# Performance work log

Measured on AMD Instinct MI355X. Metric: run time of the kernel, lower is better.

Reference implementation:

```python
import jax, jax.numpy as jnp
import numpy as np

# dims: batch, seq_len, d_model, heads, head_dim, n_buckets
B, L, DM, H, DH, K = 4, 4096, 1024, 16, 64, 8
C = L // K            # chunk length after bucket sort (512); extra_len==0 for these dims
CS = 0.1              # cluster_score mixing weight


def setup_inputs() -> dict:
    key = jax.random.key(0)
    ks = jax.random.split(key, 12)
    s = 0.02
    def p(k, shape):
        return jax.random.normal(k, shape, jnp.float32) * s
    return {
        "inputs_q": jax.random.normal(ks[0], (B, L, DM), jnp.float32),
        "wq": p(ks[1], (DM, H, DH)), "bq": jnp.zeros((H, DH), jnp.float32),
        "wk": p(ks[2], (DM, H, DH)), "bk": jnp.zeros((H, DH), jnp.float32),
        "wv": p(ks[3], (DM, H, DH)), "bv": jnp.zeros((H, DH), jnp.float32),
        "w_shared": p(ks[4], (H, DH, K)),
        "w_qscore": p(ks[5], (H, DH, K)),
        "w_kscore": p(ks[6], (H, DH, K)),
        "wo": p(ks[7], (H, DH, DM)), "bo": jnp.zeros((DM,), jnp.float32),
    }


def reference(inputs_q, wq, bq, wk, bk, wv, bv, w_shared, w_qscore, w_kscore, wo, bo):
    scale = 1.0 / np.sqrt(DH)
    # QKV projections (DenseGeneral to (H, DH))
    q = jnp.einsum('bld,dhk->blhk', inputs_q, wq) + bq  # [B,L,H,DH]
    k = jnp.einsum('bld,dhk->blhk', inputs_q, wk) + bk
    v = jnp.einsum('bld,dhk->blhk', inputs_q, wv) + bv

    # learned linear cluster scores on stop-gradient q/k
    mix_q = (1.0 - CS) * w_shared + CS * w_qscore  # [H,DH,K]
    mix_k = (1.0 - CS) * w_shared + CS * w_kscore
    qs = jnp.einsum('blhd,hdk->blhk', jax.lax.stop_gradient(q), mix_q)  # [B,L,H,K]
    ksc = jnp.einsum('blhd,hdk->blhk', jax.lax.stop_gradient(k), mix_k)

    # bucket assignment = argmax learned score; per-(batch,head) stable sort by bucket id
    bq_id = jnp.argmax(qs, -1).transpose(0, 2, 1)   # [B,H,L]
    bk_id = jnp.argmax(ksc, -1).transpose(0, 2, 1)
    sort_q = jnp.argsort(bq_id, axis=-1)            # stable in jax
    sort_k = jnp.argsort(bk_id, axis=-1)

    qh = q.transpose(0, 2, 1, 3)  # [B,H,L,DH]
    kh = k.transpose(0, 2, 1, 3)
    vh = v.transpose(0, 2, 1, 3)
    sq = jnp.take_along_axis(qh, sort_q[..., None], axis=2).reshape(B, H, K, C, DH)
    sk = jnp.take_along_axis(kh, sort_k[..., None], axis=2).reshape(B, H, K, C, DH)
    sv = jnp.take_along_axis(vh, sort_k[..., None], axis=2).reshape(B, H, K, C, DH)

    # block attention within each bucket chunk
    logits = jnp.einsum('bhncd,bhned->bhnce', sq, sk) * scale  # [B,H,K,C,C]
    attn = jax.nn.softmax(logits, axis=-1)
    o = jnp.einsum('bhnce,bhned->bhncd', attn, sv).reshape(B, H, L, DH)

    # unsort back to original token order
    inv_q = jnp.argsort(sort_q, axis=-1)
    o = jnp.take_along_axis(o, inv_q[..., None], axis=2)  # [B,H,L,DH]
    o = o.transpose(0, 2, 1, 3)                            # [B,L,H,DH]

    out = jnp.einsum('blhd,hdo->blo', o, wo) + bo          # output projection

    # auxiliary load-balancing routing loss over buckets (extra_loss)
    p_q = jax.nn.softmax(qs, -1)
    p_k = jax.nn.softmax(ksc, -1)
    f_q = jax.nn.one_hot(jnp.argmax(qs, -1), K, dtype=qs.dtype)
    f_k = jax.nn.one_hot(jnp.argmax(ksc, -1), K, dtype=qs.dtype)
    lq = K * jnp.mean(jnp.sum(jnp.mean(f_q, 1) * jnp.mean(p_q, 1), -1))
    lk = K * jnp.mean(jnp.sum(jnp.mean(f_k, 1) * jnp.mean(p_k, 1), -1))
    extra_loss = 0.5 * (lq + lk)
    return out, extra_loss
```

## Files before the change

kernel.cpp:

```cpp
#include <hip/hip_runtime.h>
#include <hip/hip_bf16.h>

#define BB 4
#define LL 4096
#define DM 1024
#define HH 16
#define DHD 64
#define KB 8
#define BL 16384
#define FLAGCAP 131072

typedef __attribute__((ext_vector_type(8))) short short8;
typedef __attribute__((ext_vector_type(4))) short short4v;
typedef __attribute__((ext_vector_type(4))) float float4v;

#define MFMA16(A, Bx, C) __builtin_amdgcn_mfma_f32_16x16x32_bf16(A, Bx, C, 0, 0, 0)

static __device__ __forceinline__ short bf16s(float f) {
  __hip_bfloat16 h = __float2bfloat16(f);
  return *reinterpret_cast<short*>(&h);
}
static __device__ __forceinline__ float b2f(short s) {
  __hip_bfloat16 h = *reinterpret_cast<__hip_bfloat16*>(&s);
  return __bfloat162float(h);
}
static __device__ __forceinline__ void gl16(const void* g, void* l) {
  __builtin_amdgcn_global_load_lds(
      (const __attribute__((address_space(1))) void*)g,
      (__attribute__((address_space(3))) void*)l, 16, 0, 0);
}

__global__ __launch_bounds__(256) void prep_wt(const float* __restrict__ wq,
                                               const float* __restrict__ wk,
                                               const float* __restrict__ wv,
                                               const float* __restrict__ wo,
                                               __hip_bfloat16* __restrict__ wt_qkv,
                                               __hip_bfloat16* __restrict__ wt_o) {
  int blk = blockIdx.x;
  int s = blk >> 8;
  int rem = blk & 255;
  int k0 = (rem >> 4) * 64;
  int n0 = (rem & 15) * 64;
  const float* src = (s == 0) ? wq : (s == 1) ? wk : (s == 2) ? wv : wo;
  __hip_bfloat16* dst = (s < 3) ? (wt_qkv + (size_t)s * 1024 * 1024) : wt_o;
  __shared__ float ls[64][65];
  int t = threadIdx.x;
#pragma unroll
  for (int p = 0; p < 4; ++p) {
    int sid = p * 256 + t;
    int r = sid >> 4, c4 = sid & 15;
    float4 v = *reinterpret_cast<const float4*>(src + (size_t)(k0 + r) * 1024 + n0 + c4 * 4);
    ls[r][c4 * 4 + 0] = v.x; ls[r][c4 * 4 + 1] = v.y;
    ls[r][c4 * 4 + 2] = v.z; ls[r][c4 * 4 + 3] = v.w;
  }
  __syncthreads();
#pragma unroll
  for (int p = 0; p < 4; ++p) {
    int sid = p * 256 + t;
    int n = sid >> 4, kq = sid & 15;
    short4v pk;
#pragma unroll
    for (int j = 0; j < 4; ++j) pk[j] = bf16s(ls[kq * 4 + j][n]);
    *reinterpret_cast<short4v*>(dst + (size_t)(n0 + n) * 1024 + k0 + kq * 4) = pk;
  }
}

__global__ __launch_bounds__(256) void prep_wsc(const float* __restrict__ wq,
                                                const float* __restrict__ wk,
                                                const float* __restrict__ wsh,
                                                const float* __restrict__ wqs,
                                                const float* __restrict__ wks,
                                                const float* __restrict__ bq,
                                                const float* __restrict__ bk,
                                                double* __restrict__ wscg,
                                                double* __restrict__ bsc,
                                                __hip_bfloat16* __restrict__ whb,
                                                __hip_bfloat16* __restrict__ wmb) {
  int col = blockIdx.x;
  int side = col >> 7, h = (col >> 3) & 15, kk = col & 7;
  int g = side * 16 + h;
  const float* w = side ? wk : wq;
  const float* wscore = side ? wks : wqs;
  __shared__ double mix[64];
  int t = threadIdx.x;
  if (t < 64)
    mix[t] = 0.9 * (double)wsh[(h * 64 + t) * 8 + kk] +
             0.1 * (double)wscore[(h * 64 + t) * 8 + kk];
  __syncthreads();
#pragma unroll
  for (int p = 0; p < 4; ++p) {
    int d = p * 256 + t;
    double acc = 0.0;
    const float* wr = w + (size_t)d * 1024 + h * 64;
#pragma unroll
    for (int j = 0; j < 64; ++j) acc += (double)wr[j] * mix[j];
    wscg[((size_t)g * 1024 + d) * 8 + kk] = acc;
    short hi = bf16s((float)acc);
    short mid = bf16s((float)(acc - (double)b2f(hi)));
    *reinterpret_cast<short*>(whb + (size_t)col * 1024 + d) = hi;
    *reinterpret_cast<short*>(wmb + (size_t)col * 1024 + d) = mid;
  }
  if (t == 0) {
    const float* br = (side ? bk : bq) + h * 64;
    double acc = 0.0;
    for (int j = 0; j < 64; ++j) acc += (double)br[j] * mix[j];
    bsc[col] = acc;
  }
}

__global__ __launch_bounds__(512) void score_gemm(const float* __restrict__ x,
                                                  const __hip_bfloat16* __restrict__ whb,
                                                  const __hip_bfloat16* __restrict__ wmb,
                                                  const double* __restrict__ bsc,
                                                  __hip_bfloat16* __restrict__ xb,
                                                  int* __restrict__ bid,
                                                  float* __restrict__ psumg,
                                                  int* __restrict__ flagcnt,
                                                  int* __restrict__ list) {
  __shared__ char sm[147456];
  int t = threadIdx.x;
  int m0 = blockIdx.x * 64;
  int lane = t & 63;
  int wu = __builtin_amdgcn_readfirstlane(t >> 6);
  int lm = lane & 15, quad = lane >> 4;
  int wmr = (wu & 1) * 32, wn = (wu >> 1) * 64;
  int rb = wu * 32, rr = lane >> 3, phys = lane & 7;
  int am = t >> 3, akc = t & 7;

  auto STAGEB = [&](int bufsel, int k0) {
    char* base = sm + 16384 + bufsel * 65536;
#pragma unroll
    for (int p = 0; p < 4; ++p) {
      int row = rb + p * 8 + rr;
      int kc = (phys - row) & 7;
      gl16(whb + (size_t)row * 1024 + k0 + kc * 8, base + (rb + p * 8) * 128);
      gl16(wmb + (size_t)row * 1024 + k0 + kc * 8, base + 32768 + (rb + p * 8) * 128);
    }
  };

  float4 xf0, xf1;
  auto LOADX = [&](int k0) {
    const float* ap = x + (size_t)(m0 + am) * 1024 + k0 + akc * 8;
    xf0 = *reinterpret_cast<const float4*>(ap);
    xf1 = *reinterpret_cast<const float4*>(ap + 4);
  };

  STAGEB(0, 0);
  LOADX(0);

  float4v zero = {0.f, 0.f, 0.f, 0.f};
  float4v acc[2][4];
#pragma unroll
  for (int i = 0; i < 2; ++i)
#pragma unroll
    for (int j = 0; j < 4; ++j) acc[i][j] = zero;

#pragma unroll 1
  for (int kt = 0; kt < 16; ++kt) {
    int k0 = kt * 64;
    short8 hi, lo;
    {
      float vv[8] = {xf0.x, xf0.y, xf0.z, xf0.w, xf1.x, xf1.y, xf1.z, xf1.w};
#pragma unroll
      for (int e = 0; e < 8; ++e) {
        short h = bf16s(vv[e]);
        hi[e] = h;
        lo[e] = bf16s(vv[e] - b2f(h));
      }
    }
    asm volatile("" ::: "memory");
    __builtin_amdgcn_s_barrier();
    asm volatile("" ::: "memory");
    *reinterpret_cast<short8*>(sm + am * 128 + ((akc + am) & 7) * 16) = hi;
    *reinterpret_cast<short8*>(sm + 8192 + am * 128 + ((akc + am) & 7) * 16) = lo;
    *reinterpret_cast<short8*>(xb + (size_t)(m0 + am) * 1024 + k0 + akc * 8) = hi;
    if (kt < 15) {
      STAGEB((kt + 1) & 1, k0 + 64);
      LOADX(k0 + 64);
    }
    asm volatile("s_waitcnt lgkmcnt(0)" ::: "memory");
    __builtin_amdgcn_s_barrier();
    asm volatile("" ::: "memory");

    const char* bb = sm + 16384 + (kt & 1) * 65536;
#pragma unroll
    for (int kh = 0; kh < 2; ++kh) {
      short8 ah[2], al[2], bh[4], bm[4];
#pragma unroll
      for (int i = 0; i < 2; ++i) {
        int row = wmr + i * 16 + lm;
        int ph = ((kh * 4 + quad) + row) & 7;
        ah[i] = *reinterpret_cast<const short8*>(sm + row * 128 + ph * 16);
        al[i] = *reinterpret_cast<const short8*>(sm + 8192 + row * 128 + ph * 16);
      }
#pragma unroll
      for (int j = 0; j < 4; ++j) {
        int rn = wn + j * 16 + lm;
        int ph = ((kh * 4 + quad) + rn) & 7;
        bh[j] = *reinterpret_cast<const short8*>(bb + rn * 128 + ph * 16);
        bm[j] = *reinterpret_cast<const short8*>(bb + 32768 + rn * 128 + ph * 16);
      }
#pragma unroll
      for (int i = 0; i < 2; ++i)
#pragma unroll
        for (int j = 0; j < 4; ++j) {
          acc[i][j] = MFMA16(ah[i], bh[j], acc[i][j]);
          acc[i][j] = MFMA16(ah[i], bm[j], acc[i][j]);
          acc[i][j] = MFMA16(al[i], bh[j], acc[i][j]);
        }
    }
  }

  int b = m0 >> 12;
  int l0 = m0 & 4095;
  int kk = lm & 7;
#pragma unroll
  for (int j = 0; j < 4; ++j) {
    int n = wn + j * 16 + lm;
    int g = n >> 3;
    int side = g >> 4, h = g & 15;
    int slab = (side * 4 + b) * 16 + h;
    float bias = (float)bsc[n];
    float pp = 0.f;
#pragma unroll
    for (int i = 0; i < 2; ++i)
#pragma unroll
      for (int r = 0; r < 4; ++r) {
        float v = acc[i][j][r] + bias;
        float bmx = v; int bi = kk;
#pragma unroll
        for (int o = 1; o < 8; o <<= 1) {
          float vo = __shfl_xor(bmx, o);
          int io = __shfl_xor(bi, o);
          if (vo > bmx || (vo == bmx && io < bi)) { bmx = vo; bi = io; }
        }
        float vm = (kk == bi) ? -3.0e38f : v;
#pragma unroll
        for (int o = 1; o < 8; o <<= 1) vm = fmaxf(vm, __shfl_xor(vm, o));
        float e = __expf(v - bmx);
        float es = e;
#pragma unroll
        for (int o = 1; o < 8; o <<= 1) es += __shfl_xor(es, o);
        pp += e * (1.f / es);
        int l = l0 + wmr + i * 16 + quad * 4 + r;
        if (kk == 0) {
          bid[(slab << 12) | l] = bi;
          if (bmx - vm < 5e-4f) {
            int pos = atomicAdd(flagcnt, 1);
            if (pos < FLAGCAP) list[pos] = (slab << 12) | l;
          }
        }
      }
    pp += __shfl_xor(pp, 16);
    pp += __shfl_xor(pp, 32);
    if (quad == 0) atomicAdd(&psumg[slab * 8 + kk], pp);
  }
}

__global__ __launch_bounds__(256) void refine_kernel(const float* __restrict__ x,
                                                     const double* __restrict__ wscg,
                                                     const double* __restrict__ bsc,
                                                     const int* __restrict__ flagcnt,
                                                     const int* __restrict__ list,
                                                     int* __restrict__ bid) {
  int lane = threadIdx.x & 63;
  int w = threadIdx.x >> 6;
  int cnt = flagcnt[0];
  if (cnt > FLAGCAP) cnt = FLAGCAP;
  for (int i = blockIdx.x * 4 + w; i < cnt; i += 1024) {
    int e = list[i];
    int slab = e >> 12, l = e & 4095;
    int side = slab >> 6, b = (slab >> 4) & 3, h = slab & 15;
    int g = side * 16 + h;
    int row = b * 4096 + l;
    double acc[8] = {0, 0, 0, 0, 0, 0, 0, 0};
    const float* xr = x + (size_t)row * 1024 + lane * 16;
    const double* wr = wscg + ((size_t)g * 1024 + lane * 16) * 8;
#pragma unroll
    for (int dd = 0; dd < 16; ++dd) {
      double xv = (double)xr[dd];
#pragma unroll
      for (int j = 0; j < 8; ++j) acc[j] += xv * wr[dd * 8 + j];
    }
#pragma unroll
    for (int j = 0; j < 8; ++j) {
      double v = acc[j];
      v += __shfl_xor(v, 32); v += __shfl_xor(v, 16); v += __shfl_xor(v, 8);
      v += __shfl_xor(v, 4);  v += __shfl_xor(v, 2);  v += __shfl_xor(v, 1);
      acc[j] = v + bsc[g * 8 + j];
    }
    if (lane == 0) {
      double mx = acc[0]; int am = 0;
#pragma unroll
      for (int j = 1; j < 8; ++j) { if (acc[j] > mx) { mx = acc[j]; am = j; } }
      bid[(slab << 12) | l] = am;
    }
  }
}

__global__ __launch_bounds__(256) void sort_kernel(const int* __restrict__ bid,
                                                   int* __restrict__ sortq,
                                                   int* __restrict__ sortk,
                                                   int* __restrict__ cntg) {
  int blk = blockIdx.x;
  int side = blk >> 6, b = (blk >> 4) & 3, h = blk & 15;
  const int* ids = bid + (((side * 4 + b) * 16 + h) << 12);
  int* outp = (side ? sortk : sortq) + ((b * 16 + h) << 12);
  __shared__ int cnt[8][257];
  __shared__ int base[8];
  int t = threadIdx.x;
  int loc[16];
  int hist[8] = {0, 0, 0, 0, 0, 0, 0, 0};
#pragma unroll
  for (int j = 0; j < 16; ++j) { loc[j] = ids[t * 16 + j] & 7; hist[loc[j]]++; }
#pragma unroll
  for (int k = 0; k < 8; ++k) cnt[k][t + 1] = hist[k];
  if (t < 8) cnt[t][0] = 0;
  __syncthreads();
  if (t < 8) {
    for (int i = 1; i <= 256; ++i) cnt[t][i] += cnt[t][i - 1];
  }
  __syncthreads();
  if (t == 0) {
    int run = 0;
    for (int k = 0; k < 8; ++k) { base[k] = run; run += cnt[k][256]; }
  }
  if (t < 8) cntg[((side * 4 + b) * 16 + h) * 8 + t] = cnt[t][256];
  __syncthreads();
#pragma unroll
  for (int j = 0; j < 16; ++j) {
    int k = loc[j];
    int before = 0;
#pragma unroll
    for (int i = 0; i < 16; ++i) before += (i < j && loc[i] == k) ? 1 : 0;
    int pos = base[k] + cnt[k][t] + before;
    outp[pos] = t * 16 + j;
  }
}

template <bool CBF16>
__global__ __launch_bounds__(512, 2) void gemm256(const __hip_bfloat16* __restrict__ A,
                                                  const __hip_bfloat16* __restrict__ Bt,
                                                  void* __restrict__ Cv,
                                                  const float* __restrict__ b0,
                                                  const float* __restrict__ b1,
                                                  const float* __restrict__ b2,
                                                  int nblk, int cpx) {
  __shared__ char sm[131072];
  int t = threadIdx.x;
  int blk = (blockIdx.x & 7) * cpx + (blockIdx.x >> 3);
  int m0 = (blk / nblk) * 256;
  int n0 = (blk % nblk) * 256;
  int lane = t & 63;
  int wu = __builtin_amdgcn_readfirstlane(t >> 6);
  int lm = lane & 15, quad = lane >> 4;
  int rr = lane >> 3, phys = lane & 7;
  int wrow = (wu & 1) * 64;
  int wcol = (wu >> 1) * 32;

  constexpr int QM[4] = {0, 0, 1, 1};
  constexpr int QN[4] = {0, 1, 1, 0};

  auto STAGE = [&](char* bufn, int j, int kS) {
    const int mat = (j == 1 || j == 2) ? 1 : 0;
    const int hm = (j >= 2) ? 1 : 0;
    const __hip_bfloat16* src = mat ? Bt : A;
    int gb = mat ? n0 : m0;
    char* lb = bufn + mat * 32768 + hm * 16384;
#pragma unroll
    for (int i = 0; i < 2; ++i) {
      int r = hm * 128 + (wu * 2 + i) * 8 + rr;
      int kc = (phys - r) & 7;
      gl16(src + (size_t)(gb + r) * 1024 + kS + kc * 8, lb + (wu * 2 + i) * 1024);
    }
  };

#pragma unroll
  for (int j = 0; j < 4; ++j) STAGE(sm, j, 0);

  float4v zero = {0.f, 0.f, 0.f, 0.f};
  float4v acc[4][4][2];
#pragma unroll
  for (int q = 0; q < 4; ++q)
#pragma unroll
    for (int mi = 0; mi < 4; ++mi)
#pragma unroll
      for (int ni = 0; ni < 2; ++ni) acc[q][mi][ni] = zero;

  short8 a[4][2], b[2][2];
  auto READA = [&](const char* bc, int qm) {
#pragma unroll
    for (int mi = 0; mi < 4; ++mi) {
      int row = qm * 128 + wrow + mi * 16 + lm;
#pragma unroll
      for (int ks = 0; ks < 2; ++ks) {
        int ph = ((ks * 4 + quad) + row) & 7;
        a[mi][ks] = *reinterpret_cast<const short8*>(bc + row * 128 + ph * 16);
      }
    }
  };
  auto READB = [&](const char* bc, int qn) {
#pragma unroll
    for (int ni = 0; ni < 2; ++ni) {
      int rn = qn * 128 + wcol + ni * 16 + lm;
#pragma unroll
      for (int ks = 0; ks < 2; ++ks) {
        int ph = ((ks * 4 + quad) + rn) & 7;
        b[ni][ks] = *reinterpret_cast<const short8*>(bc + 32768 + rn * 128 + ph * 16);
      }
    }
  };

#pragma unroll 1
  for (int kt = 0; kt < 16; ++kt) {
    char* bc = sm + ((kt & 1) << 16);
    char* bn = sm + (((kt & 1) ^ 1) << 16);
    int kS = (kt < 15) ? (kt + 1) * 64 : 960;
#pragma unroll
    for (int j = 0; j < 4; ++j) {
      if (j < 3) {
        asm volatile("s_waitcnt vmcnt(4)" ::: "memory");
        __builtin_amdgcn_s_barrier();
      }
      if (j == 0) { READA(bc, 0); READB(bc, 0); }
      else if (j == 1) { READB(bc, 1); }
      else if (j == 2) { READA(bc, 1); }
      else { READB(bc, 0); }
      STAGE(bn, j, kS);
      __builtin_amdgcn_s_setprio(1);
#pragma unroll
      for (int mi = 0; mi < 4; ++mi)
#pragma unroll
        for (int ni = 0; ni < 2; ++ni)
#pragma unroll
          for (int ks = 0; ks < 2; ++ks)
            acc[j][mi][ni] = MFMA16(a[mi][ks], b[ni][ks], acc[j][mi][ni]);
      __builtin_amdgcn_s_setprio(0);
    }
  }
  asm volatile("s_waitcnt vmcnt(0)" ::: "memory");

  if constexpr (CBF16) {
#pragma unroll
    for (int j = 0; j < 4; ++j)
#pragma unroll
      for (int mi = 0; mi < 4; ++mi)
#pragma unroll
        for (int ni = 0; ni < 2; ++ni) {
          int nn = n0 + QN[j] * 128 + wcol + ni * 16 + lm;
          int s = nn >> 10, nnb = nn & 1023;
          const float* bias = (s == 0) ? b0 : (s == 1) ? b1 : b2;
          float bvx = bias[nnb];
          __hip_bfloat16* C = (__hip_bfloat16*)Cv + (size_t)s * BL * 1024;
#pragma unroll
          for (int r = 0; r < 4; ++r) {
            int row = m0 + QM[j] * 128 + wrow + mi * 16 + quad * 4 + r;
            C[(size_t)row * 1024 + nnb] = __float2bfloat16(acc[j][mi][ni][r] + bvx);
          }
        }
  } else {
    float* C = (float*)Cv;
#pragma unroll
    for (int j = 0; j < 4; ++j)
#pragma unroll
      for (int mi = 0; mi < 4; ++mi)
#pragma unroll
        for (int ni = 0; ni < 2; ++ni) {
          int nn = n0 + QN[j] * 128 + wcol + ni * 16 + lm;
          float bvx = b0[nn];
#pragma unroll
          for (int r = 0; r < 4; ++r) {
            int row = m0 + QM[j] * 128 + wrow + mi * 16 + quad * 4 + r;
            C[(size_t)row * 1024 + nn] = acc[j][mi][ni][r] + bvx;
          }
        }
  }
}

__global__ __launch_bounds__(256) void vt_kernel(const __hip_bfloat16* __restrict__ vb,
                                                 const int* __restrict__ sortk,
                                                 __hip_bfloat16* __restrict__ vT) {
  int cid = blockIdx.x;
  int b = cid >> 7, h = (cid >> 3) & 15, n = cid & 7;
  int sbase = ((b * 16 + h) << 12) + n * 512;
  __shared__ __hip_bfloat16 ls[64][72];
  int t = threadIdx.x;
  for (int kt = 0; kt < 8; ++kt) {
    __syncthreads();
#pragma unroll
    for (int p = 0; p < 2; ++p) {
      int sid = p * 256 + t;
      int key = sid >> 3, kc = sid & 7;
      int tok = sortk[sbase + kt * 64 + key];
      short8 v = *reinterpret_cast<const short8*>(vb + ((size_t)(b * 4096 + tok) * 16 + h) * 64 + kc * 8);
      *reinterpret_cast<short8*>(&ls[key][kc * 8]) = v;
    }
    __syncthreads();
#pragma unroll
    for (int p = 0; p < 2; ++p) {
      int sid = p * 256 + t;
      int dim = sid >> 3, kc = sid & 7;
      short8 o;
#pragma unroll
      for (int j = 0; j < 8; ++j) o[j] = *reinterpret_cast<short*>(&ls[kc * 8 + j][dim]);
      *reinterpret_cast<short8*>(vT + ((size_t)cid * 64 + dim) * 512 + kt * 64 + kc * 8) = o;
    }
  }
}

__global__ __launch_bounds__(512, 2) void attn_kernel(const __hip_bfloat16* __restrict__ qb,
                                                      const __hip_bfloat16* __restrict__ kb,
                                                      const __hip_bfloat16* __restrict__ vT,
                                                      const int* __restrict__ sortq,
                                                      const int* __restrict__ sortk,
                                                      __hip_bfloat16* __restrict__ ao) {
  __shared__ char sm[149504];
  int t = threadIdx.x;
  int lane = t & 63, w = t >> 6;
  int lm = lane & 15, quad = lane >> 4;
  int cid = blockIdx.x;
  int b = cid >> 7, h = (cid >> 3) & 15, n = cid & 7;
  int sbase = (b * 16 + h) << 12;
  int psOff = 131072 + w * 2304;

  {
    int row = t >> 3, kc = t & 7;
    int sw = ((kc + row) & 7) * 16;
#pragma unroll
    for (int kt = 0; kt < 8; ++kt) {
      int tok = sortk[sbase + n * 512 + kt * 64 + row];
      short8 kv = *reinterpret_cast<const short8*>(
          kb + ((size_t)(b * 4096 + tok) * 16 + h) * 64 + kc * 8);
      *reinterpret_cast<short8*>(sm + kt * 8192 + row * 128 + sw) = kv;
      short8 vv = *reinterpret_cast<const short8*>(
          vT + ((size_t)cid * 64 + row) * 512 + kt * 64 + kc * 8);
      *reinterpret_cast<short8*>(sm + 65536 + kt * 8192 + row * 128 + sw) = vv;
    }
  }
  __syncthreads();

  float4v zero = {0.f, 0.f, 0.f, 0.f};
#pragma unroll 1
  for (int qr = 0; qr < 4; ++qr) {
    int qtok = sortq[sbase + n * 512 + qr * 128 + w * 16 + lm];
    const __hip_bfloat16* qp = qb + ((size_t)(b * 4096 + qtok) * 16 + h) * 64 + quad * 8;
    short8 aq0 = *reinterpret_cast<const short8*>(qp);
    short8 aq1 = *reinterpret_cast<const short8*>(qp + 32);

    float4v accO[4];
#pragma unroll
    for (int i = 0; i < 4; ++i) accO[i] = zero;
    float lsum[4] = {0.f, 0.f, 0.f, 0.f};

#pragma unroll 1
    for (int kt = 0; kt < 8; ++kt) {
      const char* Kt = sm + kt * 8192;
      const char* Vt = sm + 65536 + kt * 8192;
#pragma unroll
      for (int nt = 0; nt < 4; ++nt) {
        int key = nt * 16 + lm;
        int ph0 = (quad + key) & 7;
        int ph1 = (4 + quad + key) & 7;
        short8 bk0 = *reinterpret_cast<const short8*>(Kt + key * 128 + ph0 * 16);
        short8 bk1 = *reinterpret_cast<const short8*>(Kt + key * 128 + ph1 * 16);
        float4v S = zero;
        S = MFMA16(aq0, bk0, S);
        S = MFMA16(aq1, bk1, S);
#pragma unroll
        for (int r = 0; r < 4; ++r) {
          float e = __expf(S[r] * 0.125f);
          lsum[r] += e;
          *reinterpret_cast<short*>(sm + psOff + (quad * 4 + r) * 144 + key * 2) = bf16s(e);
        }
      }
      __builtin_amdgcn_s_waitcnt(0);
#pragma unroll
      for (int ks = 0; ks < 2; ++ks) {
        short8 ap = *reinterpret_cast<const short8*>(sm + psOff + lm * 144 + ks * 64 + quad * 16);
#pragma unroll
        for (int dt = 0; dt < 4; ++dt) {
          int dim = dt * 16 + lm;
          int ph = (ks * 4 + quad + dim) & 7;
          short8 bv = *reinterpret_cast<const short8*>(Vt + dim * 128 + ph * 16);
          accO[dt] = MFMA16(ap, bv, accO[dt]);
        }
      }
    }
#pragma unroll
    for (int r = 0; r < 4; ++r) {
      float l = lsum[r];
      l += __shfl_xor(l, 1); l += __shfl_xor(l, 2);
      l += __shfl_xor(l, 4); l += __shfl_xor(l, 8);
      lsum[r] = 1.f / l;
    }
#pragma unroll
    for (int dt = 0; dt < 4; ++dt)
#pragma unroll
      for (int r = 0; r < 4; ++r)
        *reinterpret_cast<short*>(sm + psOff + (quad * 4 + r) * 144 + (dt * 16 + lm) * 2) =
            bf16s(accO[dt][r] * lsum[r]);
    __builtin_amdgcn_s_waitcnt(0);
    int q2 = lane >> 2, c = lane & 3;
    int tok2 = sortq[sbase + n * 512 + qr * 128 + w * 16 + q2];
    __hip_bfloat16* op = ao + ((size_t)(b * 4096 + tok2) * 16 + h) * 64;
    short8 o0 = *reinterpret_cast<const short8*>(sm + psOff + q2 * 144 + c * 16);
    short8 o1 = *reinterpret_cast<const short8*>(sm + psOff + q2 * 144 + (c + 4) * 16);
    *reinterpret_cast<short8*>(op + c * 8) = o0;
    *reinterpret_cast<short8*>(op + (c + 4) * 8) = o1;
  }
}

__global__ __launch_bounds__(1024) void loss_kernel(const int* __restrict__ cntg,
                                                    const float* __restrict__ psumg,
                                                    float* __restrict__ out) {
  int t = threadIdx.x;
  float term = ((float)cntg[t] * (1.f / 4096.f)) * (psumg[t] * (1.f / 4096.f));
#pragma unroll
  for (int o = 1; o < 64; o <<= 1) term += __shfl_xor(term, o);
  __shared__ float wsum[16];
  if ((t & 63) == 0) wsum[t >> 6] = term;
  __syncthreads();
  if (t == 0) {
    float s = 0.f;
    for (int i = 0; i < 16; ++i) s += wsum[i];
    out[16777216] = s * (1.f / 16.f);
  }
}

extern "C" void kernel_launch(void* const* d_in, const int* in_sizes, int n_in,
                              void* d_out, int out_size, void* d_ws, size_t ws_size,
                              hipStream_t stream) {
  (void)in_sizes; (void)n_in; (void)out_size; (void)ws_size;
  const float* x   = (const float*)d_in[0];
  const float* wq  = (const float*)d_in[1];
  const float* bq  = (const float*)d_in[2];
  const float* wk  = (const float*)d_in[3];
  const float* bk  = (const float*)d_in[4];
  const float* wv  = (const float*)d_in[5];
  const float* bv  = (const float*)d_in[6];
  const float* wsh = (const float*)d_in[7];
  const float* wqs = (const float*)d_in[8];
  const float* wks = (const float*)d_in[9];
  const float* wo  = (const float*)d_in[10];
  const float* bo  = (const float*)d_in[11];

  char* ws = (char*)d_ws;
  __hip_bfloat16* wt_qkv = (__hip_bfloat16*)(ws + 0);
  __hip_bfloat16* wt_o   = (__hip_bfloat16*)(ws + 6291456);
  double* wscg  = (double*)(ws + 8388608);
  double* bsc   = (double*)(ws + 10485760);
  __hip_bfloat16* qkv  = (__hip_bfloat16*)(ws + 10487808);
  __hip_bfloat16* whb = (__hip_bfloat16*)(ws + 109051904);
  __hip_bfloat16* wmb = (__hip_bfloat16*)(ws + 109576192);
  int* flagcnt = (int*)(ws + 110100480);
  int* list    = (int*)(ws + 110100736);
  __hip_bfloat16* attn = (__hip_bfloat16*)(ws + 111151104);
  int* bid    = (int*)(ws + 144705536);
  int* sortq  = (int*)(ws + 146802688);
  int* sortk  = (int*)(ws + 147851264);
  float* psumg = (float*)(ws + 148899840);
  int* cntg    = (int*)(ws + 148903936);
  __hip_bfloat16* vT = (__hip_bfloat16*)d_out;
  __hip_bfloat16* xb = (__hip_bfloat16*)((char*)d_out + 33554432);
  float* out = (float*)d_out;

  hipMemsetAsync(psumg, 0, 8192, stream);
  hipMemsetAsync(flagcnt, 0, 4, stream);
  prep_wt<<<1024, 256, 0, stream>>>(wq, wk, wv, wo, wt_qkv, wt_o);
  prep_wsc<<<256, 256, 0, stream>>>(wq, wk, wsh, wqs, wks, bq, bk, wscg, bsc, whb, wmb);
  score_gemm<<<256, 512, 0, stream>>>(x, whb, wmb, bsc, xb, bid, psumg, flagcnt, list);
  refine_kernel<<<256, 256, 0, stream>>>(x, wscg, bsc, flagcnt, list, bid);
  sort_kernel<<<128, 256, 0, stream>>>(bid, sortq, sortk, cntg);
  gemm256<true><<<768, 512, 0, stream>>>(xb, wt_qkv, qkv, bq, bk, bv, 12, 96);
  vt_kernel<<<512, 256, 0, stream>>>(qkv + (size_t)2 * BL * 1024, sortk, vT);
  attn_kernel<<<512, 512, 0, stream>>>(qkv, qkv + (size_t)BL * 1024, vT, sortq, sortk, attn);
  gemm256<false><<<256, 512, 0, stream>>>(attn, wt_o, (void*)out, bo, bo, bo, 4, 32);
  loss_kernel<<<1, 1024, 0, stream>>>(cntg, psumg, out);
}
```

Before: 526.5 us.

## Split x bf16 hi/lo conversion out of score GEMM and retile into 128x128 pipelined blocks

Adds a standalone kernel that converts x into bf16 hi and lo planes, so the score GEMM no longer converts fp32 x inline. The score GEMM is retiled from 64-row x 256-col blocks to 128x128 tiles and stages all four operands (x hi, w hi, w mid, x lo) with async global-to-LDS loads. Those loads are interleaved with three MFMA phases per k-step, using partial vmcnt waits and setprio. The cost is an extra kernel launch and a round trip of x hi/lo through memory, plus doubled x traffic per output tile.

```diff
diff --git a/kernel.cpp b/kernel.cpp
--- a/kernel.cpp
+++ b/kernel.cpp
@@ -28,6 +28,24 @@
   __builtin_amdgcn_global_load_lds(
       (const __attribute__((address_space(1))) void*)g,
       (__attribute__((address_space(3))) void*)l, 16, 0, 0);
+}
+
+__global__ __launch_bounds__(256) void xcvt2(const float* __restrict__ x,
+                                             __hip_bfloat16* __restrict__ xh,
+                                             __hip_bfloat16* __restrict__ xl) {
+  int i = (blockIdx.x * 256 + threadIdx.x) * 8;
+  float4 f0 = *reinterpret_cast<const float4*>(x + i);
+  float4 f1 = *reinterpret_cast<const float4*>(x + i + 4);
+  float vv[8] = {f0.x, f0.y, f0.z, f0.w, f1.x, f1.y, f1.z, f1.w};
+  short8 hi, lo;
+#pragma unroll
+  for (int e = 0; e < 8; ++e) {
+    short h = bf16s(vv[e]);
+    hi[e] = h;
+    lo[e] = bf16s(vv[e] - b2f(h));
+  }
+  *reinterpret_cast<short8*>(xh + i) = hi;
+  *reinterpret_cast<short8*>(xl + i) = lo;
 }
 
 __global__ __launch_bounds__(256) void prep_wt(const float* __restrict__ wq,
@@ -108,125 +126,125 @@
   }
 }
 
-__global__ __launch_bounds__(512) void score_gemm(const float* __restrict__ x,
-                                                  const __hip_bfloat16* __restrict__ whb,
-                                                  const __hip_bfloat16* __restrict__ wmb,
-                                                  const double* __restrict__ bsc,
-                                                  __hip_bfloat16* __restrict__ xb,
-                                                  int* __restrict__ bid,
-                                                  float* __restrict__ psumg,
-                                                  int* __restrict__ flagcnt,
-                                                  int* __restrict__ list) {
-  __shared__ char sm[147456];
-  int t = threadIdx.x;
-  int m0 = blockIdx.x * 64;
+__global__ __launch_bounds__(512, 2) void score_gemm(const __hip_bfloat16* __restrict__ xh,
+                                                     const __hip_bfloat16* __restrict__ xl,
+                                                     const __hip_bfloat16* __restrict__ whb,
+                                                     const __hip_bfloat16* __restrict__ wmb,
+                                                     const double* __restrict__ bsc,
+                                                     int* __restrict__ bid,
+                                                     float* __restrict__ psumg,
+                                                     int* __restrict__ flagcnt,
+                                                     int* __restrict__ list) {
+  __shared__ char sm[131072];
+  int t = threadIdx.x;
+  int blk = (blockIdx.x & 7) * 32 + (blockIdx.x >> 3);
+  int m0 = (blk >> 1) * 128;
+  int n0 = (blk & 1) * 128;
   int lane = t & 63;
   int wu = __builtin_amdgcn_readfirstlane(t >> 6);
   int lm = lane & 15, quad = lane >> 4;
-  int wmr = (wu & 1) * 32, wn = (wu >> 1) * 64;
-  int rb = wu * 32, rr = lane >> 3, phys = lane & 7;
-  int am = t >> 3, akc = t & 7;
-
-  auto STAGEB = [&](int bufsel, int k0) {
-    char* base = sm + 16384 + bufsel * 65536;
-#pragma unroll
-    for (int p = 0; p < 4; ++p) {
-      int row = rb + p * 8 + rr;
-      int kc = (phys - row) & 7;
-      gl16(whb + (size_t)row * 1024 + k0 + kc * 8, base + (rb + p * 8) * 128);
-      gl16(wmb + (size_t)row * 1024 + k0 + kc * 8, base + 32768 + (rb + p * 8) * 128);
+  int rr = lane >> 3, phys = lane & 7;
+  int wrow = (wu & 1) * 64;
+  int wcol = (wu >> 1) * 32;
+
+  auto STAGE = [&](char* bufn, int u, int kS) {
+    const __hip_bfloat16* src = (u == 0) ? xh : (u == 1) ? whb : (u == 2) ? wmb : xl;
+    int gb = (u == 1 || u == 2) ? n0 : m0;
+    char* lb = bufn + u * 16384;
+#pragma unroll
+    for (int i = 0; i < 2; ++i) {
+      int r = (wu * 2 + i) * 8 + rr;
+      int kc = (phys - r) & 7;
+      gl16(src + (size_t)(gb + r) * 1024 + kS + kc * 8, lb + (wu * 2 + i) * 1024);
     }
   };
 
-  float4 xf0, xf1;
-  auto LOADX = [&](int k0) {
-    const float* ap = x + (size_t)(m0 + am) * 1024 + k0 + akc * 8;
-    xf0 = *reinterpret_cast<const float4*>(ap);
-    xf1 = *reinterpret_cast<const float4*>(ap + 4);
+  STAGE(sm, 0, 0); STAGE(sm, 1, 0); STAGE(sm, 2, 0); STAGE(sm, 3, 0);
+
+  float4v zero = {0.f, 0.f, 0.f, 0.f};
+  float4v acc[4][2];
+#pragma unroll
+  for (int mi = 0; mi < 4; ++mi)
+#pragma unroll
+    for (int ni = 0; ni < 2; ++ni) acc[mi][ni] = zero;
+
+  short8 ahi[4][2], alo[4][2], bwh[2][2], bwm[2][2];
+  auto READA = [&](short8 (&aa)[4][2], const char* base) {
+#pragma unroll
+    for (int mi = 0; mi < 4; ++mi) {
+      int row = wrow + mi * 16 + lm;
+#pragma unroll
+      for (int ks = 0; ks < 2; ++ks) {
+        int ph = ((ks * 4 + quad) + row) & 7;
+        aa[mi][ks] = *reinterpret_cast<const short8*>(base + row * 128 + ph * 16);
+      }
+    }
   };
-
-  STAGEB(0, 0);
-  LOADX(0);
-
-  float4v zero = {0.f, 0.f, 0.f, 0.f};
-  float4v acc[2][4];
-#pragma unroll
-  for (int i = 0; i < 2; ++i)
-#pragma unroll
-    for (int j = 0; j < 4; ++j) acc[i][j] = zero;
+  auto READB = [&](short8 (&bb)[2][2], const char* base) {
+#pragma unroll
+    for (int ni = 0; ni < 2; ++ni) {
+      int rn = wcol + ni * 16 + lm;
+#pragma unroll
+      for (int ks = 0; ks < 2; ++ks) {
+        int ph = ((ks * 4 + quad) + rn) & 7;
+        bb[ni][ks] = *reinterpret_cast<const short8*>(base + rn * 128 + ph * 16);
+      }
+    }
+  };
+
+#define SMFMA(AA, BB)                                                        \
+  __builtin_amdgcn_s_setprio(1);                                             \
+  _Pragma("unroll") for (int mi = 0; mi < 4; ++mi)                           \
+      _Pragma("unroll") for (int ni = 0; ni < 2; ++ni)                       \
+          _Pragma("unroll") for (int ks = 0; ks < 2; ++ks)                   \
+              acc[mi][ni] = MFMA16(AA[mi][ks], BB[ni][ks], acc[mi][ni]);     \
+  __builtin_amdgcn_s_setprio(0);
 
 #pragma unroll 1
   for (int kt = 0; kt < 16; ++kt) {
-    int k0 = kt * 64;
-    short8 hi, lo;
-    {
-      float vv[8] = {xf0.x, xf0.y, xf0.z, xf0.w, xf1.x, xf1.y, xf1.z, xf1.w};
-#pragma unroll
-      for (int e = 0; e < 8; ++e) {
-        short h = bf16s(vv[e]);
-        hi[e] = h;
-        lo[e] = bf16s(vv[e] - b2f(h));
-      }
-    }
-    asm volatile("" ::: "memory");
+    char* bc = sm + ((kt & 1) << 16);
+    char* bn = sm + (((kt & 1) ^ 1) << 16);
+    int kS = (kt < 15) ? (kt + 1) * 64 : 960;
+
+    asm volatile("s_waitcnt vmcnt(4)" ::: "memory");
     __builtin_amdgcn_s_barrier();
-    asm volatile("" ::: "memory");
-    *reinterpret_cast<short8*>(sm + am * 128 + ((akc + am) & 7) * 16) = hi;
-    *reinterpret_cast<short8*>(sm + 8192 + am * 128 + ((akc + am) & 7) * 16) = lo;
-    *reinterpret_cast<short8*>(xb + (size_t)(m0 + am) * 1024 + k0 + akc * 8) = hi;
-    if (kt < 15) {
-      STAGEB((kt + 1) & 1, k0 + 64);
-      LOADX(k0 + 64);
-    }
-    asm volatile("s_waitcnt lgkmcnt(0)" ::: "memory");
+    READA(ahi, bc);
+    READB(bwh, bc + 16384);
+    STAGE(bn, 0, kS);
+    SMFMA(ahi, bwh)
+
+    asm volatile("s_waitcnt vmcnt(4)" ::: "memory");
     __builtin_amdgcn_s_barrier();
-    asm volatile("" ::: "memory");
-
-    const char* bb = sm + 16384 + (kt & 1) * 65536;
-#pragma unroll
-    for (int kh = 0; kh < 2; ++kh) {
-      short8 ah[2], al[2], bh[4], bm[4];
-#pragma unroll
-      for (int i = 0; i < 2; ++i) {
-        int row = wmr + i * 16 + lm;
-        int ph = ((kh * 4 + quad) + row) & 7;
-        ah[i] = *reinterpret_cast<const short8*>(sm + row * 128 + ph * 16);
-        al[i] = *reinterpret_cast<const short8*>(sm + 8192 + row * 128 + ph * 16);
-      }
-#pragma unroll
-      for (int j = 0; j < 4; ++j) {
-        int rn = wn + j * 16 + lm;
-        int ph = ((kh * 4 + quad) + rn) & 7;
-        bh[j] = *reinterpret_cast<const short8*>(bb + rn * 128 + ph * 16);
-        bm[j] = *reinterpret_cast<const short8*>(bb + 32768 + rn * 128 + ph * 16);
-      }
-#pragma unroll
-      for (int i = 0; i < 2; ++i)
-#pragma unroll
-        for (int j = 0; j < 4; ++j) {
-          acc[i][j] = MFMA16(ah[i], bh[j], acc[i][j]);
-          acc[i][j] = MFMA16(ah[i], bm[j], acc[i][j]);
-          acc[i][j] = MFMA16(al[i], bh[j], acc[i][j]);
-        }
-    }
-  }
+    READB(bwm, bc + 32768);
+    STAGE(bn, 1, kS);
+    SMFMA(ahi, bwm)
+
+    asm volatile("s_waitcnt vmcnt(4)" ::: "memory");
+    __builtin_amdgcn_s_barrier();
+    READA(alo, bc + 49152);
+    STAGE(bn, 2, kS);
+    STAGE(bn, 3, kS);
+    SMFMA(alo, bwh)
+  }
+  asm volatile("s_waitcnt vmcnt(0)" ::: "memory");
+#undef SMFMA
 
   int b = m0 >> 12;
   int l0 = m0 & 4095;
   int kk = lm & 7;
 #pragma unroll
-  for (int j = 0; j < 4; ++j) {
-    int n = wn + j * 16 + lm;
+  for (int ni = 0; ni < 2; ++ni) {
+    int n = n0 + wcol + ni * 16 + lm;
     int g = n >> 3;
     int side = g >> 4, h = g & 15;
     int slab = (side * 4 + b) * 16 + h;
     float bias = (float)bsc[n];
     float pp = 0.f;
 #pragma unroll
-    for (int i = 0; i < 2; ++i)
+    for (int mi = 0; mi < 4; ++mi)
 #pragma unroll
       for (int r = 0; r < 4; ++r) {
-        float v = acc[i][j][r] + bias;
+        float v = acc[mi][ni][r] + bias;
         float bmx = v; int bi = kk;
 #pragma unroll
         for (int o = 1; o < 8; o <<= 1) {
@@ -242,7 +260,7 @@
 #pragma unroll
         for (int o = 1; o < 8; o <<= 1) es += __shfl_xor(es, o);
         pp += e * (1.f / es);
-        int l = l0 + wmr + i * 16 + quad * 4 + r;
+        int l = l0 + wrow + mi * 16 + quad * 4 + r;
         if (kk == 0) {
           bid[(slab << 12) | l] = bi;
           if (bmx - vm < 5e-4f) {
@@ -660,6 +678,7 @@
   int* sortk  = (int*)(ws + 147851264);
   float* psumg = (float*)(ws + 148899840);
   int* cntg    = (int*)(ws + 148903936);
+  __hip_bfloat16* xl = (__hip_bfloat16*)d_out;
   __hip_bfloat16* vT = (__hip_bfloat16*)d_out;
   __hip_bfloat16* xb = (__hip_bfloat16*)((char*)d_out + 33554432);
   float* out = (float*)d_out;
@@ -668,7 +687,8 @@
   hipMemsetAsync(flagcnt, 0, 4, stream);
   prep_wt<<<1024, 256, 0, stream>>>(wq, wk, wv, wo, wt_qkv, wt_o);
   prep_wsc<<<256, 256, 0, stream>>>(wq, wk, wsh, wqs, wks, bq, bk, wscg, bsc, whb, wmb);
-  score_gemm<<<256, 512, 0, stream>>>(x, whb, wmb, bsc, xb, bid, psumg, flagcnt, list);
+  xcvt2<<<8192, 256, 0, stream>>>(x, xb, xl);
+  score_gemm<<<256, 512, 0, stream>>>(xb, xl, whb, wmb, bsc, bid, psumg, flagcnt, list);
   refine_kernel<<<256, 256, 0, stream>>>(x, wscg, bsc, flagcnt, list, bid);
   sort_kernel<<<128, 256, 0, stream>>>(bid, sortq, sortk, cntg);
   gemm256<true><<<768, 512, 0, stream>>>(xb, wt_qkv, qkv, bq, bk, bv, 12, 96);
```

Result: no change. 517.0 us (-1.8%).
